# Optimization experiments

Measured on AMD Instinct MI355X. Metric: run time of the kernel, lower is better.

## Reference

```python
import jax, jax.numpy as jnp
import numpy as np

L, N, K, S, V, H = 12, 2048, 8, 4, 50000, 256


def setup_inputs() -> dict:
    key = jax.random.key(0)
    ks = jax.random.split(key, 20)
    tokens1 = jax.random.randint(ks[0], (L, N, S), 0, V, dtype=jnp.int32)
    tokens2 = jax.random.randint(ks[1], (L, N, S), 0, V, dtype=jnp.int32)
    # child indices into previous level's h (0 = zero-init row, -1 = no child)
    idx1 = jax.random.randint(ks[2], (L, N, K), -1, N + 1, dtype=jnp.int32).at[0].set(-1)
    idx2 = jax.random.randint(ks[3], (L, N, K), -1, N + 1, dtype=jnp.int32).at[0].set(-1)
    sc = 0.02
    E = jax.random.normal(ks[4], (V, H), jnp.float32)  # torch.randn init
    lin_W = jax.random.normal(ks[5], (H * S, H), jnp.float32) * sc
    lin_b = jnp.zeros((H,), jnp.float32)
    Uf_W = jax.random.normal(ks[6], (H, H), jnp.float32) * sc
    Uf_b = jnp.zeros((H,), jnp.float32)
    Uiuo_W = jax.random.normal(ks[7], (H, 3 * H), jnp.float32) * sc
    Uiuo_b = jnp.zeros((3 * H,), jnp.float32)
    W_W = jax.random.normal(ks[8], (H, 4 * H), jnp.float32) * sc
    W_b = jnp.zeros((4 * H,), jnp.float32)
    dense_W = jax.random.normal(ks[9], (H, 512), jnp.float32) * sc
    dense_b = jnp.zeros((512,), jnp.float32)
    out_W = jax.random.normal(ks[10], (512, 2), jnp.float32) * sc
    out_b = jnp.zeros((2,), jnp.float32)
    return dict(tokens1=tokens1, idx1=idx1, tokens2=tokens2, idx2=idx2,
                E=E, lin_W=lin_W, lin_b=lin_b, Uf_W=Uf_W, Uf_b=Uf_b,
                Uiuo_W=Uiuo_W, Uiuo_b=Uiuo_b, W_W=W_W, W_b=W_b,
                dense_W=dense_W, dense_b=dense_b, out_W=out_W, out_b=out_b)


def _encode(tokens, idx, E, lin_W, lin_b, Uf_W, Uf_b, Uiuo_W, Uiuo_b, W_W, W_b):
    # TreeEmbeddingLayer: lookup label_size tokens per node, concat, linear
    emb = E[tokens].reshape(L, N, S * H)           # [L,N,S*H]
    x = emb @ lin_W + lin_b                        # [L,N,H]

    def step(carry, inp):
        h_prev, c_prev = carry                     # [N,H]
        xl, il = inp                               # [N,H], [N,K]
        zero = jnp.zeros((1, H), xl.dtype)
        hp = jnp.concatenate([zero, h_prev], 0)    # [N+1,H] (row 0 = init)
        cp = jnp.concatenate([zero, c_prev], 0)
        mask_bool = il != -1
        index = jnp.where(mask_bool, il, 0)
        h = hp[index]                              # [N,K,H] gather child states
        c = cp[index]
        m = mask_bool[..., None].astype(xl.dtype)  # [N,K,1]
        h_sum = jnp.sum(h * m, axis=1)             # [N,H]
        Wx = xl @ W_W + W_b                        # [N,4H]
        Wf, Wi, Wu, Wo = Wx[:, :H], Wx[:, H:2*H], Wx[:, 2*H:3*H], Wx[:, 3*H:]
        fk = jax.nn.sigmoid(Wf[:, None, :] + h @ Uf_W + Uf_b)  # [N,K,H]
        bf = jnp.sum(fk * c * m, axis=1)           # [N,H]
        iuo = h_sum @ Uiuo_W + Uiuo_b              # [N,3H]
        i = jax.nn.sigmoid(iuo[:, :H] + Wi)
        u = jnp.tanh(iuo[:, H:2*H] + Wu)
        o = jax.nn.sigmoid(iuo[:, 2*H:] + Wo)
        nc = i * u + bf
        nh = o * jnp.tanh(nc)
        return (nh, nc), nh

    init = (jnp.zeros((N, H), x.dtype), jnp.zeros((N, H), x.dtype))
    (_, _), hs = jax.lax.scan(step, init, (x, idx))
    # 1 layer with skip connection; hx = last (root) level
    return hs[-1] + x[-1]                          # [N,H]


def reference(tokens1, idx1, tokens2, idx2, E, lin_W, lin_b, Uf_W, Uf_b,
              Uiuo_W, Uiuo_b, W_W, W_b, dense_W, dense_b, out_W, out_b):
    h1 = _encode(tokens1, idx1, E, lin_W, lin_b, Uf_W, Uf_b, Uiuo_W, Uiuo_b, W_W, W_b)
    h2 = _encode(tokens2, idx2, E, lin_W, lin_b, Uf_W, Uf_b, Uiuo_W, Uiuo_b, W_W, W_b)
    abs_dist = jnp.abs(h1 - h2)                    # [N,H]
    x = jnp.tanh(abs_dist @ dense_W + dense_b)     # dropout = identity (eval)
    logits = x @ out_W + out_b                     # [N,2]
    return jax.nn.softmax(logits, axis=-1)
```

## Files before the change

kernel.cpp:

```cpp
#include <hip/hip_runtime.h>

#define LL 12
#define NN 2048
#define KK 8
#define SS 4
#define HH 256
#define LN (LL*NN)
#define VV 50000
#define ZROW 4096
#define SROW 1536

typedef __bf16 bf16_t;
typedef __bf16 bf16x8 __attribute__((ext_vector_type(8)));
typedef __bf16 bf16x4v __attribute__((ext_vector_type(4)));
typedef float f32x4 __attribute__((ext_vector_type(4)));

__device__ __forceinline__ float sigmoidf_(float x) { return 1.f / (1.f + expf(-x)); }

__global__ __launch_bounds__(256) void k_cvtE(const float* __restrict__ src,
                                              bf16_t* __restrict__ dst, int n4)
{
    int i = blockIdx.x * 256 + threadIdx.x;
    const int stride = gridDim.x * 256;
    for (; i < n4; i += stride) {
        const float4 v = ((const float4*)src)[i];
        bf16x4v o;
        o[0] = (bf16_t)v.x; o[1] = (bf16_t)v.y; o[2] = (bf16_t)v.z; o[3] = (bf16_t)v.w;
        ((bf16x4v*)dst)[i] = o;
    }
}

__global__ __launch_bounds__(256) void k_cvtW(
    const float* __restrict__ linW, const float* __restrict__ WW,
    const float* __restrict__ UfW, const float* __restrict__ UiW,
    bf16_t* __restrict__ linWt, bf16_t* __restrict__ WWt,
    bf16_t* __restrict__ UfWt, bf16_t* __restrict__ UiWt)
{
    int i = blockIdx.x * 256 + threadIdx.x;
    if (i < 262144) {
        const int rr = i >> 8, cc = i & 255;
        linWt[(size_t)cc * 1024 + rr] = (bf16_t)linW[i];
        return;
    }
    i -= 262144;
    if (i < 262144) {
        const int rr = i >> 10, cc = i & 1023;
        WWt[(size_t)cc * 256 + rr] = (bf16_t)WW[i];
        return;
    }
    i -= 262144;
    if (i < 65536) {
        const int rr = i >> 8, cc = i & 255;
        UfWt[(size_t)cc * 256 + rr] = (bf16_t)UfW[i];
        return;
    }
    i -= 65536;
    if (i < 196608) {
        const int rr = i / 768, cc = i - rr * 768;
        UiWt[(size_t)cc * 256 + rr] = (bf16_t)UiW[i];
    }
}

__global__ __launch_bounds__(256) void k_zero(float* __restrict__ SA, float* __restrict__ SB)
{
    const int t = threadIdx.x;
    float* a = SA + (size_t)ZROW * 384;
    float* b = SB + (size_t)ZROW * 384;
    for (int i = t; i < 384; i += 256) { a[i] = 0.f; b[i] = 0.f; }
}

__global__ __launch_bounds__(256) void k_embedwx(
    const int* __restrict__ tok1, const int* __restrict__ tok2,
    const bf16_t* __restrict__ Ebf, const bf16_t* __restrict__ linWt,
    const float* __restrict__ linb,
    const bf16_t* __restrict__ WWt, const float* __restrict__ Wb,
    bf16_t* __restrict__ xsm, bf16_t* __restrict__ Wxs)
{
    __shared__ int toff[64][SS];
    __shared__ __align__(16) bf16_t xtile[64 * 256];
    const int t = threadIdx.x;
    const int m0 = blockIdx.x * 64;
    {
        const int lr = t >> 2, s = t & 3;
        const int m = m0 + lr;
        const int e = (m >= LN) ? 1 : 0;
        const int rrow = m - e * LN;
        const int* tok = e ? tok2 : tok1;
        toff[lr][s] = tok[(size_t)rrow * SS + s] * HH;
    }
    __syncthreads();
    const int lane = t & 63, w = t >> 6;
    const int wm = w >> 1, wn = w & 1;
    const int r = lane & 15, kg = lane >> 4;
    const int lr0 = wm * 32 + r, lr1 = lr0 + 16;
    const f32x4 zero = {0.f, 0.f, 0.f, 0.f};

    {
        const bf16_t* bp[8];
        #pragma unroll
        for (int j = 0; j < 8; ++j)
            bp[j] = linWt + (size_t)(wn * 128 + j * 16 + r) * 1024 + kg * 8;
        f32x4 acc[2][8];
        #pragma unroll
        for (int mi = 0; mi < 2; ++mi)
            #pragma unroll
            for (int j = 0; j < 8; ++j) acc[mi][j] = zero;

        for (int k0 = 0; k0 < 1024; k0 += 32) {
            const int s = k0 >> 8, off = (k0 & 255) + kg * 8;
            const bf16x8 a0 = *(const bf16x8*)(Ebf + (size_t)toff[lr0][s] + off);
            const bf16x8 a1 = *(const bf16x8*)(Ebf + (size_t)toff[lr1][s] + off);
            #pragma unroll
            for (int j = 0; j < 8; ++j) {
                const bf16x8 b = *(const bf16x8*)bp[j];
                acc[0][j] = __builtin_amdgcn_mfma_f32_16x16x32_bf16(a0, b, acc[0][j], 0, 0, 0);
                acc[1][j] = __builtin_amdgcn_mfma_f32_16x16x32_bf16(a1, b, acc[1][j], 0, 0, 0);
                bp[j] += 32;
            }
        }
        const int e0 = (m0 >= LN) ? 1 : 0;
        const int lblk = (m0 - e0 * LN) >> 11;
        const int nbase = m0 & (NN - 1);
        const int crowL = wm * 32 + kg * 4;
        #pragma unroll
        for (int j = 0; j < 8; ++j) {
            const int ccol = wn * 128 + j * 16 + r;
            const float bv = linb[ccol];
            #pragma unroll
            for (int mi = 0; mi < 2; ++mi) {
                #pragma unroll
                for (int jj = 0; jj < 4; ++jj) {
                    const int rowL = crowL + mi * 16 + jj;
                    const bf16_t val = (bf16_t)(acc[mi][j][jj] + bv);
                    const int ps = ((ccol >> 3) + rowL) & 31;
                    xtile[rowL * 256 + ps * 8 + (ccol & 7)] = val;
                    if (lblk == LL - 1)
                        xsm[((size_t)e0 * NN + nbase + rowL) * HH + ccol] = val;
                }
            }
        }
    }
    __syncthreads();

    for (int mp = 0; mp < 2; ++mp) {
        for (int nh = 0; nh < 2; ++nh) {
            f32x4 acc2[2][8];
            #pragma unroll
            for (int mi = 0; mi < 2; ++mi)
                #pragma unroll
                for (int nt = 0; nt < 8; ++nt) acc2[mi][nt] = zero;
            for (int k0 = 0; k0 < 8; ++k0) {
                const int row0 = mp * 32 + r, row1 = row0 + 16;
                const int sk = k0 * 4 + kg;
                const bf16x8 a0 = *(const bf16x8*)(xtile + row0 * 256 + ((sk + row0) & 31) * 8);
                const bf16x8 a1 = *(const bf16x8*)(xtile + row1 * 256 + ((sk + row1) & 31) * 8);
                #pragma unroll
                for (int nt = 0; nt < 8; ++nt) {
                    const bf16x8 b = *(const bf16x8*)(WWt +
                        (size_t)(w * 256 + (nh * 8 + nt) * 16 + r) * HH + k0 * 32 + kg * 8);
                    acc2[0][nt] = __builtin_amdgcn_mfma_f32_16x16x32_bf16(a0, b, acc2[0][nt], 0, 0, 0);
                    acc2[1][nt] = __builtin_amdgcn_mfma_f32_16x16x32_bf16(a1, b, acc2[1][nt], 0, 0, 0);
                }
            }
            #pragma unroll
            for (int nt = 0; nt < 8; ++nt) {
                const int col = w * 256 + (nh * 8 + nt) * 16 + r;
                const float bv = Wb[col];
                #pragma unroll
                for (int mi = 0; mi < 2; ++mi) {
                    #pragma unroll
                    for (int jj = 0; jj < 4; ++jj)
                        Wxs[(size_t)(m0 + mp * 32 + mi * 16 + kg * 4 + jj) * 1024 + col] =
                            (bf16_t)(acc2[mi][nt][jj] + bv);
                }
            }
        }
    }
}

__global__ __launch_bounds__(512, 2) void k_step2(
    const int* __restrict__ idx1, const int* __restrict__ idx2, const int l,
    const bf16_t* __restrict__ UfWt, const float* __restrict__ Ufb,
    const bf16_t* __restrict__ UiWt, const float* __restrict__ Uib,
    const bf16_t* __restrict__ Wxs,
    const char* __restrict__ Sprev, char* __restrict__ Snext)
{
    __shared__ __align__(16) bf16_t iuoL[16 * 768];
    __shared__ __align__(16) bf16_t hsumL[16 * 256];

    const int t = threadIdx.x;
    const int bid = blockIdx.x;
    const int x  = bid & 7;
    const int e  = x >> 2;
    const int n0 = ((bid >> 3) * 4 + (x & 3)) * 16;
    const int g0 = e * NN + n0;
    const int lane = t & 63, w = t >> 6;
    const int r = lane & 15, kg = lane >> 4;
    const f32x4 zero = {0.f, 0.f, 0.f, 0.f};

    const int rr = t >> 5, sl = t & 31;
    const int ss = (sl + 4 * (rr & 7)) & 31;

    int ch[KK];
    {
        const int* idxp = (e ? idx2 : idx1) + ((size_t)l * NN + n0 + rr) * KK;
        const int4 i0 = *(const int4*)idxp;
        const int4 i1 = *(const int4*)(idxp + 4);
        ch[0] = i0.x; ch[1] = i0.y; ch[2] = i0.z; ch[3] = i0.w;
        ch[4] = i1.x; ch[5] = i1.y; ch[6] = i1.z; ch[7] = i1.w;
        #pragma unroll
        for (int k = 0; k < KK; ++k)
            ch[k] = (ch[k] >= 1) ? (e * NN + ch[k] - 1) : ZROW;
    }

    const bf16_t* wxp = Wxs + ((size_t)e * LN + (size_t)l * NN + n0 + rr) * 1024;
    const bf16x8 wfv = *(const bf16x8*)(wxp + sl * 8);
    const bf16x8 wiv = *(const bf16x8*)(wxp + 256 + sl * 8);
    const bf16x8 wuv = *(const bf16x8*)(wxp + 512 + sl * 8);
    const bf16x8 wov = *(const bf16x8*)(wxp + 768 + sl * 8);
    bf16x8 hv[KK], fv[KK], cv[KK];
    #pragma unroll
    for (int k = 0; k < KK; ++k) {
        const char* row = Sprev + (size_t)ch[k] * SROW;
        hv[k] = *(const bf16x8*)(row + sl * 16);
        fv[k] = *(const bf16x8*)(row + 512 + sl * 16);
        cv[k] = *(const bf16x8*)(row + 1024 + sl * 16);
    }

    {
        float hs[8] = {0.f, 0.f, 0.f, 0.f, 0.f, 0.f, 0.f, 0.f};
        #pragma unroll
        for (int k = 0; k < KK; ++k) {
            #pragma unroll
            for (int j = 0; j < 8; ++j) hs[j] += (float)hv[k][j];
        }
        bf16x8 o;
        #pragma unroll
        for (int j = 0; j < 8; ++j) o[j] = (bf16_t)hs[j];
        *(bf16x8*)(hsumL + rr * 256 + ss * 8) = o;
    }
    __syncthreads();

    {
        const bf16_t* bu[6];
        #pragma unroll
        for (int j = 0; j < 6; ++j)
            bu[j] = UiWt + (size_t)((6 * w + j) * 16 + r) * HH + kg * 8;
        f32x4 acc[6];
        #pragma unroll
        for (int j = 0; j < 6; ++j) acc[j] = zero;
        for (int k0 = 0; k0 < HH; k0 += 32) {
            const int sa = (((k0 >> 3) + kg) + 4 * (r & 7)) & 31;
            const bf16x8 a = *(const bf16x8*)(hsumL + r * 256 + sa * 8);
            #pragma unroll
            for (int j = 0; j < 6; ++j) {
                const bf16x8 b = *(const bf16x8*)bu[j];
                acc[j] = __builtin_amdgcn_mfma_f32_16x16x32_bf16(a, b, acc[j], 0, 0, 0);
                bu[j] += 32;
            }
        }
        #pragma unroll
        for (int j = 0; j < 6; ++j) {
            const int col = (6 * w + j) * 16 + r;
            const float bv = Uib[col];
            #pragma unroll
            for (int jj = 0; jj < 4; ++jj)
                iuoL[(size_t)(kg * 4 + jj) * 768 + col] = (bf16_t)(acc[j][jj] + bv);
        }
    }

    float ba[8] = {0.f, 0.f, 0.f, 0.f, 0.f, 0.f, 0.f, 0.f};
    {
        float wf[8];
        #pragma unroll
        for (int j = 0; j < 8; ++j) wf[j] = (float)wfv[j];
        #pragma unroll
        for (int k = 0; k < KK; ++k) {
            #pragma unroll
            for (int j = 0; j < 8; ++j) {
                const float fk = sigmoidf_(wf[j] + (float)fv[k][j]);
                ba[j] = fmaf(fk, (float)cv[k][j], ba[j]);
            }
        }
    }
    __syncthreads();

    {
        const bf16x8 iv = *(const bf16x8*)(iuoL + (size_t)rr * 768 + sl * 8);
        const bf16x8 uv = *(const bf16x8*)(iuoL + (size_t)rr * 768 + 256 + sl * 8);
        const bf16x8 ov = *(const bf16x8*)(iuoL + (size_t)rr * 768 + 512 + sl * 8);
        bf16x8 ncb, nhb;
        #pragma unroll
        for (int j = 0; j < 8; ++j) {
            const float ig = sigmoidf_((float)iv[j] + (float)wiv[j]);
            const float ug = tanhf((float)uv[j] + (float)wuv[j]);
            const float og = sigmoidf_((float)ov[j] + (float)wov[j]);
            const float nc = fmaf(ig, ug, ba[j]);
            ncb[j] = (bf16_t)nc;
            nhb[j] = (bf16_t)(og * tanhf(nc));
        }
        char* rowN = Snext + (size_t)(g0 + rr) * SROW;
        *(bf16x8*)(rowN + sl * 16) = nhb;
        *(bf16x8*)(rowN + 1024 + sl * 16) = ncb;
        *(bf16x8*)(hsumL + rr * 256 + ss * 8) = nhb;
    }

    if (l < LL - 1) {
        __syncthreads();
        const int ct0 = 2 * w;
        const bf16_t* bq0 = UfWt + (size_t)(ct0 * 16 + r) * HH + kg * 8;
        const bf16_t* bq1 = bq0 + (size_t)16 * HH;
        f32x4 ac0 = zero, ac1 = zero;
        for (int k0 = 0; k0 < HH; k0 += 32) {
            const int sa = (((k0 >> 3) + kg) + 4 * (r & 7)) & 31;
            const bf16x8 a = *(const bf16x8*)(hsumL + r * 256 + sa * 8);
            const bf16x8 b0 = *(const bf16x8*)bq0;
            const bf16x8 b1 = *(const bf16x8*)bq1;
            ac0 = __builtin_amdgcn_mfma_f32_16x16x32_bf16(a, b0, ac0, 0, 0, 0);
            ac1 = __builtin_amdgcn_mfma_f32_16x16x32_bf16(a, b1, ac1, 0, 0, 0);
            bq0 += 32; bq1 += 32;
        }
        const int c0 = ct0 * 16 + r, c1 = c0 + 16;
        const float bv0 = Ufb[c0], bv1 = Ufb[c1];
        #pragma unroll
        for (int jj = 0; jj < 4; ++jj) {
            bf16_t* fr = (bf16_t*)(Snext + (size_t)(g0 + kg * 4 + jj) * SROW + 512);
            fr[c0] = (bf16_t)(ac0[jj] + bv0);
            fr[c1] = (bf16_t)(ac1[jj] + bv1);
        }
    }
}

__global__ __launch_bounds__(256) void k_final2(
    const char* __restrict__ Sfin, const bf16_t* __restrict__ xsm,
    const float* __restrict__ dW, const float* __restrict__ db,
    const float* __restrict__ oW, const float* __restrict__ ob,
    float* __restrict__ out)
{
    __shared__ __align__(16) float ad[8][HH];
    __shared__ __align__(16) float xx[8][512];
    const int t = threadIdx.x;
    const int n0 = blockIdx.x * 8;
    #pragma unroll
    for (int rr = 0; rr < 8; ++rr) {
        const int n = n0 + rr;
        const float h1 = (float)((const bf16_t*)(Sfin + (size_t)n * SROW))[t]
                       + (float)xsm[(size_t)n * HH + t];
        const float h2 = (float)((const bf16_t*)(Sfin + (size_t)(NN + n) * SROW))[t]
                       + (float)xsm[((size_t)NN + n) * HH + t];
        ad[rr][t] = fabsf(h1 - h2);
    }
    __syncthreads();
    float a0[8], a1[8];
    #pragma unroll
    for (int rr = 0; rr < 8; ++rr) { a0[rr] = 0.f; a1[rr] = 0.f; }
    for (int k = 0; k < HH; k += 4) {
        #pragma unroll
        for (int kk = 0; kk < 4; ++kk) {
            const float b0 = dW[(size_t)(k + kk) * 512 + t];
            const float b1 = dW[(size_t)(k + kk) * 512 + 256 + t];
            #pragma unroll
            for (int rr = 0; rr < 8; ++rr) {
                const float av = ad[rr][k + kk];
                a0[rr] = fmaf(av, b0, a0[rr]);
                a1[rr] = fmaf(av, b1, a1[rr]);
            }
        }
    }
    const float db0 = db[t], db1 = db[256 + t];
    #pragma unroll
    for (int rr = 0; rr < 8; ++rr) {
        xx[rr][t] = tanhf(a0[rr] + db0);
        xx[rr][256 + t] = tanhf(a1[rr] + db1);
    }
    __syncthreads();
    const int w = t >> 6, lane = t & 63;
    for (int rr = w; rr < 8; rr += 4) {
        float p0 = 0.f, p1 = 0.f;
        for (int k = lane; k < 512; k += 64) {
            const float xv = xx[rr][k];
            p0 = fmaf(xv, oW[2 * k + 0], p0);
            p1 = fmaf(xv, oW[2 * k + 1], p1);
        }
        #pragma unroll
        for (int off = 32; off > 0; off >>= 1) {
            p0 += __shfl_down(p0, off);
            p1 += __shfl_down(p1, off);
        }
        if (lane == 0) {
            const float l0 = p0 + ob[0], l1 = p1 + ob[1];
            const float mx = fmaxf(l0, l1);
            const float e0 = expf(l0 - mx), e1 = expf(l1 - mx);
            const float inv = 1.f / (e0 + e1);
            out[(size_t)(n0 + rr) * 2 + 0] = e0 * inv;
            out[(size_t)(n0 + rr) * 2 + 1] = e1 * inv;
        }
    }
}

__global__ __launch_bounds__(256) void k_embed(
    const int* __restrict__ tok1, const int* __restrict__ tok2,
    const bf16_t* __restrict__ Ebf, const bf16_t* __restrict__ linWt,
    const float* __restrict__ linb, bf16_t* __restrict__ xout)
{
    __shared__ int toff[64][SS];
    const int t = threadIdx.x;
    const int m0 = blockIdx.x * 64;
    {
        const int lr = t >> 2, s = t & 3;
        const int m = m0 + lr;
        const int e = (m >= LN) ? 1 : 0;
        const int rrow = m - e * LN;
        const int* tok = e ? tok2 : tok1;
        toff[lr][s] = tok[(size_t)rrow * SS + s] * HH;
    }
    __syncthreads();
    const int lane = t & 63, w = t >> 6;
    const int wm = w >> 1, wn = w & 1;
    const int r = lane & 15, kg = lane >> 4;
    const int lr0 = wm * 32 + r, lr1 = lr0 + 16;
    const bf16_t* bp[8];
    #pragma unroll
    for (int j = 0; j < 8; ++j)
        bp[j] = linWt + (size_t)(wn * 128 + j * 16 + r) * 1024 + kg * 8;
    const f32x4 zero = {0.f, 0.f, 0.f, 0.f};
    f32x4 acc[2][8];
    #pragma unroll
    for (int mi = 0; mi < 2; ++mi)
        #pragma unroll
        for (int j = 0; j < 8; ++j) acc[mi][j] = zero;
    for (int k0 = 0; k0 < 1024; k0 += 32) {
        const int s = k0 >> 8, off = (k0 & 255) + kg * 8;
        const bf16x8 a0 = *(const bf16x8*)(Ebf + (size_t)toff[lr0][s] + off);
        const bf16x8 a1 = *(const bf16x8*)(Ebf + (size_t)toff[lr1][s] + off);
        #pragma unroll
        for (int j = 0; j < 8; ++j) {
            const bf16x8 b = *(const bf16x8*)bp[j];
            acc[0][j] = __builtin_amdgcn_mfma_f32_16x16x32_bf16(a0, b, acc[0][j], 0, 0, 0);
            acc[1][j] = __builtin_amdgcn_mfma_f32_16x16x32_bf16(a1, b, acc[1][j], 0, 0, 0);
            bp[j] += 32;
        }
    }
    const int crow = m0 + wm * 32 + kg * 4;
    #pragma unroll
    for (int j = 0; j < 8; ++j) {
        const int ccol = wn * 128 + j * 16 + r;
        const float bv = linb[ccol];
        #pragma unroll
        for (int mi = 0; mi < 2; ++mi)
            #pragma unroll
            for (int jj = 0; jj < 4; ++jj)
                xout[(size_t)(crow + mi * 16 + jj) * HH + ccol] =
                    (bf16_t)(acc[mi][j][jj] + bv);
    }
}

__global__ __launch_bounds__(512, 2) void k_step(
    const bf16_t* __restrict__ xbf,
    const int* __restrict__ idx1, const int* __restrict__ idx2, const int l,
    const bf16_t* __restrict__ UfWt, const float* __restrict__ Ufb,
    const bf16_t* __restrict__ UiWt, const float* __restrict__ Uib,
    const bf16_t* __restrict__ WWt, const float* __restrict__ Wb,
    const char* __restrict__ Sprev, char* __restrict__ Snext)
{
    __shared__ __align__(16) bf16_t WxL[16 * 1024];
    __shared__ __align__(16) bf16_t iuoL[16 * 768];
    __shared__ __align__(16) bf16_t hsumL[16 * 256];
    const int t = threadIdx.x;
    const int bid = blockIdx.x;
    const int x  = bid & 7;
    const int e  = x >> 2;
    const int n0 = ((bid >> 3) * 4 + (x & 3)) * 16;
    const int g0 = e * NN + n0;
    const int lane = t & 63, w = t >> 6;
    const int r = lane & 15, kg = lane >> 4;
    const f32x4 zero = {0.f, 0.f, 0.f, 0.f};
    const int rr = t >> 5, sl = t & 31;
    const int ss = (sl + 4 * (rr & 7)) & 31;
    int ch[KK];
    {
        const int* idxp = (e ? idx2 : idx1) + ((size_t)l * NN + n0 + rr) * KK;
        const int4 i0 = *(const int4*)idxp;
        const int4 i1 = *(const int4*)(idxp + 4);
        ch[0] = i0.x; ch[1] = i0.y; ch[2] = i0.z; ch[3] = i0.w;
        ch[4] = i1.x; ch[5] = i1.y; ch[6] = i1.z; ch[7] = i1.w;
        #pragma unroll
        for (int k = 0; k < KK; ++k)
            ch[k] = (ch[k] >= 1) ? (e * NN + ch[k] - 1) : ZROW;
    }
    bf16x8 hv[KK];
    #pragma unroll
    for (int k = 0; k < KK; ++k)
        hv[k] = *(const bf16x8*)(Sprev + (size_t)ch[k] * SROW + sl * 16);
    const bf16_t* xrow = xbf + ((size_t)e * LN + (size_t)l * NN + n0 + r) * HH + kg * 8;
    bf16x8 aWx[8];
    #pragma unroll
    for (int k = 0; k < 8; ++k) aWx[k] = *(const bf16x8*)(xrow + k * 32);
    {
        const bf16_t* bw[8];
        #pragma unroll
        for (int j = 0; j < 8; ++j)
            bw[j] = WWt + (size_t)((8 * w + j) * 16 + r) * HH + kg * 8;
        f32x4 acc[8];
        #pragma unroll
        for (int j = 0; j < 8; ++j) acc[j] = zero;
        #pragma unroll
        for (int k = 0; k < 8; ++k) {
            #pragma unroll
            for (int j = 0; j < 8; ++j) {
                const bf16x8 b = *(const bf16x8*)bw[j];
                acc[j] = __builtin_amdgcn_mfma_f32_16x16x32_bf16(aWx[k], b, acc[j], 0, 0, 0);
                bw[j] += 32;
            }
        }
        #pragma unroll
        for (int j = 0; j < 8; ++j) {
            const int col = (8 * w + j) * 16 + r;
            const float bv = Wb[col];
            #pragma unroll
            for (int jj = 0; jj < 4; ++jj)
                WxL[(size_t)(kg * 4 + jj) * 1024 + col] = (bf16_t)(acc[j][jj] + bv);
        }
    }
    {
        float hs[8] = {0.f, 0.f, 0.f, 0.f, 0.f, 0.f, 0.f, 0.f};
        #pragma unroll
        for (int k = 0; k < KK; ++k) {
            #pragma unroll
            for (int j = 0; j < 8; ++j) hs[j] += (float)hv[k][j];
        }
        bf16x8 o;
        #pragma unroll
        for (int j = 0; j < 8; ++j) o[j] = (bf16_t)hs[j];
        *(bf16x8*)(hsumL + rr * 256 + ss * 8) = o;
    }
    __syncthreads();
    bf16x8 cv[KK], fvv[KK];
    #pragma unroll
    for (int k = 0; k < KK; ++k) {
        const char* row = Sprev + (size_t)ch[k] * SROW;
        fvv[k] = *(const bf16x8*)(row + 512 + sl * 16);
        cv[k]  = *(const bf16x8*)(row + 1024 + sl * 16);
    }
    {
        const bf16_t* bu[6];
        #pragma unroll
        for (int j = 0; j < 6; ++j)
            bu[j] = UiWt + (size_t)((6 * w + j) * 16 + r) * HH + kg * 8;
        f32x4 acc[6];
        #pragma unroll
        for (int j = 0; j < 6; ++j) acc[j] = zero;
        for (int k0 = 0; k0 < HH; k0 += 32) {
            const int sa = (((k0 >> 3) + kg) + 4 * (r & 7)) & 31;
            const bf16x8 a = *(const bf16x8*)(hsumL + r * 256 + sa * 8);
            #pragma unroll
            for (int j = 0; j < 6; ++j) {
                const bf16x8 b = *(const bf16x8*)bu[j];
                acc[j] = __builtin_amdgcn_mfma_f32_16x16x32_bf16(a, b, acc[j], 0, 0, 0);
                bu[j] += 32;
            }
        }
        #pragma unroll
        for (int j = 0; j < 6; ++j) {
            const int col = (6 * w + j) * 16 + r;
            const float bv = Uib[col];
            #pragma unroll
            for (int jj = 0; jj < 4; ++jj)
                iuoL[(size_t)(kg * 4 + jj) * 768 + col] = (bf16_t)(acc[j][jj] + bv);
        }
    }
    float ba[8] = {0.f, 0.f, 0.f, 0.f, 0.f, 0.f, 0.f, 0.f};
    {
        float wf[8];
        const bf16x8 wv = *(const bf16x8*)(WxL + (size_t)rr * 1024 + sl * 8);
        #pragma unroll
        for (int j = 0; j < 8; ++j) wf[j] = (float)wv[j];
        #pragma unroll
        for (int k = 0; k < KK; ++k) {
            #pragma unroll
            for (int j = 0; j < 8; ++j) {
                const float fk = sigmoidf_(wf[j] + (float)fvv[k][j]);
                ba[j] = fmaf(fk, (float)cv[k][j], ba[j]);
            }
        }
    }
    __syncthreads();
    {
        const bf16x8 wiv = *(const bf16x8*)(WxL + (size_t)rr * 1024 + 256 + sl * 8);
        const bf16x8 wuv = *(const bf16x8*)(WxL + (size_t)rr * 1024 + 512 + sl * 8);
        const bf16x8 wov = *(const bf16x8*)(WxL + (size_t)rr * 1024 + 768 + sl * 8);
        const bf16x8 iv  = *(const bf16x8*)(iuoL + (size_t)rr * 768 + sl * 8);
        const bf16x8 uv  = *(const bf16x8*)(iuoL + (size_t)rr * 768 + 256 + sl * 8);
        const bf16x8 ov  = *(const bf16x8*)(iuoL + (size_t)rr * 768 + 512 + sl * 8);
        bf16x8 ncb, nhb;
        #pragma unroll
        for (int j = 0; j < 8; ++j) {
            const float ig = sigmoidf_((float)iv[j] + (float)wiv[j]);
            const float ug = tanhf((float)uv[j] + (float)wuv[j]);
            const float og = sigmoidf_((float)ov[j] + (float)wov[j]);
            const float nc = fmaf(ig, ug, ba[j]);
            ncb[j] = (bf16_t)nc;
            nhb[j] = (bf16_t)(og * tanhf(nc));
        }
        char* rowN = Snext + (size_t)(g0 + rr) * SROW;
        *(bf16x8*)(rowN + sl * 16) = nhb;
        *(bf16x8*)(rowN + 1024 + sl * 16) = ncb;
        *(bf16x8*)(hsumL + rr * 256 + ss * 8) = nhb;
    }
    if (l < LL - 1) {
        __syncthreads();
        const int ct0 = 2 * w;
        const bf16_t* bq0 = UfWt + (size_t)(ct0 * 16 + r) * HH + kg * 8;
        const bf16_t* bq1 = bq0 + (size_t)16 * HH;
        f32x4 ac0 = zero, ac1 = zero;
        for (int k0 = 0; k0 < HH; k0 += 32) {
            const int sa = (((k0 >> 3) + kg) + 4 * (r & 7)) & 31;
            const bf16x8 a = *(const bf16x8*)(hsumL + r * 256 + sa * 8);
            const bf16x8 b0 = *(const bf16x8*)bq0;
            const bf16x8 b1 = *(const bf16x8*)bq1;
            ac0 = __builtin_amdgcn_mfma_f32_16x16x32_bf16(a, b0, ac0, 0, 0, 0);
            ac1 = __builtin_amdgcn_mfma_f32_16x16x32_bf16(a, b1, ac1, 0, 0, 0);
            bq0 += 32; bq1 += 32;
        }
        const int c0 = ct0 * 16 + r, c1 = c0 + 16;
        const float bv0 = Ufb[c0], bv1 = Ufb[c1];
        #pragma unroll
        for (int jj = 0; jj < 4; ++jj) {
            bf16_t* fr = (bf16_t*)(Snext + (size_t)(g0 + kg * 4 + jj) * SROW + 512);
            fr[c0] = (bf16_t)(ac0[jj] + bv0);
            fr[c1] = (bf16_t)(ac1[jj] + bv1);
        }
    }
}

__global__ __launch_bounds__(256) void k_final(
    const char* __restrict__ Sfin, const bf16_t* __restrict__ xbf,
    const float* __restrict__ dW, const float* __restrict__ db,
    const float* __restrict__ oW, const float* __restrict__ ob,
    float* __restrict__ out)
{
    __shared__ __align__(16) float ad[8][HH];
    __shared__ __align__(16) float xx[8][512];
    const int t = threadIdx.x;
    const int n0 = blockIdx.x * 8;
    const size_t xoff1 = (size_t)(LL - 1) * NN * HH;
    const size_t xoff2 = (size_t)LN * HH + xoff1;
    #pragma unroll
    for (int rr = 0; rr < 8; ++rr) {
        const int n = n0 + rr;
        const float h1 = (float)((const bf16_t*)(Sfin + (size_t)n * SROW))[t]
                       + (float)xbf[xoff1 + (size_t)n * HH + t];
        const float h2 = (float)((const bf16_t*)(Sfin + (size_t)(NN + n) * SROW))[t]
                       + (float)xbf[xoff2 + (size_t)n * HH + t];
        ad[rr][t] = fabsf(h1 - h2);
    }
    __syncthreads();
    float a0[8], a1[8];
    #pragma unroll
    for (int rr = 0; rr < 8; ++rr) { a0[rr] = 0.f; a1[rr] = 0.f; }
    for (int k = 0; k < HH; k += 4) {
        #pragma unroll
        for (int kk = 0; kk < 4; ++kk) {
            const float b0 = dW[(size_t)(k + kk) * 512 + t];
            const float b1 = dW[(size_t)(k + kk) * 512 + 256 + t];
            #pragma unroll
            for (int rr = 0; rr < 8; ++rr) {
                const float av = ad[rr][k + kk];
                a0[rr] = fmaf(av, b0, a0[rr]);
                a1[rr] = fmaf(av, b1, a1[rr]);
            }
        }
    }
    const float db0 = db[t], db1 = db[256 + t];
    #pragma unroll
    for (int rr = 0; rr < 8; ++rr) {
        xx[rr][t] = tanhf(a0[rr] + db0);
        xx[rr][256 + t] = tanhf(a1[rr] + db1);
    }
    __syncthreads();
    const int w = t >> 6, lane = t & 63;
    for (int rr = w; rr < 8; rr += 4) {
        float p0 = 0.f, p1 = 0.f;
        for (int k = lane; k < 512; k += 64) {
            const float xv = xx[rr][k];
            p0 = fmaf(xv, oW[2 * k + 0], p0);
            p1 = fmaf(xv, oW[2 * k + 1], p1);
        }
        #pragma unroll
        for (int off = 32; off > 0; off >>= 1) {
            p0 += __shfl_down(p0, off);
            p1 += __shfl_down(p1, off);
        }
        if (lane == 0) {
            const float l0 = p0 + ob[0], l1 = p1 + ob[1];
            const float mx = fmaxf(l0, l1);
            const float e0 = expf(l0 - mx), e1 = expf(l1 - mx);
            const float inv = 1.f / (e0 + e1);
            out[(size_t)(n0 + rr) * 2 + 0] = e0 * inv;
            out[(size_t)(n0 + rr) * 2 + 1] = e1 * inv;
        }
    }
}

extern "C" void kernel_launch(void* const* d_in, const int* in_sizes, int n_in,
                              void* d_out, int out_size, void* d_ws, size_t ws_size,
                              hipStream_t stream) {
    (void)in_sizes; (void)n_in; (void)out_size;
    const int*   tok1 = (const int*)d_in[0];
    const int*   idx1 = (const int*)d_in[1];
    const int*   tok2 = (const int*)d_in[2];
    const int*   idx2 = (const int*)d_in[3];
    const float* E    = (const float*)d_in[4];
    const float* linW = (const float*)d_in[5];
    const float* linb = (const float*)d_in[6];
    const float* UfW  = (const float*)d_in[7];
    const float* Ufb  = (const float*)d_in[8];
    const float* UiW  = (const float*)d_in[9];
    const float* Uib  = (const float*)d_in[10];
    const float* WW   = (const float*)d_in[11];
    const float* Wb   = (const float*)d_in[12];
    const float* dW   = (const float*)d_in[13];
    const float* db   = (const float*)d_in[14];
    const float* oW   = (const float*)d_in[15];
    const float* ob   = (const float*)d_in[16];
    float* out = (float*)d_out;

    const size_t NEED = 100663296ull + 25600000ull + 2097152ull + 1572864ull;

    if (ws_size >= NEED) {
        bf16_t* Wxs = (bf16_t*)d_ws;
        char*   uni = (char*)d_ws + 100663296;
        bf16_t* Ebf = (bf16_t*)uni;
        char*   SA  = uni;
        char*   SB  = uni + 6292992;
        bf16_t* xsm = (bf16_t*)(uni + 25600000);
        bf16_t* linWt = (bf16_t*)(uni + 25600000 + 2097152);
        bf16_t* WWt   = linWt + (size_t)262144;
        bf16_t* UfWt  = WWt   + (size_t)262144;
        bf16_t* UiWt  = UfWt  + (size_t)65536;

        k_cvtE<<<2048, 256, 0, stream>>>(E, Ebf, VV * HH / 4);
        k_cvtW<<<3072, 256, 0, stream>>>(linW, WW, UfW, UiW, linWt, WWt, UfWt, UiWt);
        k_embedwx<<<768, 256, 0, stream>>>(tok1, tok2, Ebf, linWt, linb, WWt, Wb, xsm, Wxs);
        k_zero<<<1, 256, 0, stream>>>((float*)SA, (float*)SB);

        char *Sp = SA, *Sn = SB;
        for (int l = 0; l < LL; ++l) {
            k_step2<<<256, 512, 0, stream>>>(idx1, idx2, l, UfWt, Ufb, UiWt, Uib,
                                             Wxs, Sp, Sn);
            char* ts = Sp; Sp = Sn; Sn = ts;
        }
        k_final2<<<NN / 8, 256, 0, stream>>>(Sp, xsm, dW, db, oW, ob, out);
    } else {
        bf16_t* xbf = (bf16_t*)d_ws;
        char*   uni = (char*)(xbf + (size_t)12582912);
        bf16_t* Ebf = (bf16_t*)uni;
        char*   SA  = uni;
        char*   SB  = uni + 6292992;
        bf16_t* linWt = (bf16_t*)(uni + 25600000);
        bf16_t* WWt   = linWt + (size_t)262144;
        bf16_t* UfWt  = WWt   + (size_t)262144;
        bf16_t* UiWt  = UfWt  + (size_t)65536;

        k_cvtE<<<2048, 256, 0, stream>>>(E, Ebf, VV * HH / 4);
        k_cvtW<<<3072, 256, 0, stream>>>(linW, WW, UfW, UiW, linWt, WWt, UfWt, UiWt);
        k_embed<<<768, 256, 0, stream>>>(tok1, tok2, Ebf, linWt, linb, xbf);
        k_zero<<<1, 256, 0, stream>>>((float*)SA, (float*)SB);

        char *Sp = SA, *Sn = SB;
        for (int l = 0; l < LL; ++l) {
            k_step<<<256, 512, 0, stream>>>(xbf, idx1, idx2, l,
                                            UfWt, Ufb, UiWt, Uib, WWt, Wb, Sp, Sn);
            char* ts = Sp; Sp = Sn; Sn = ts;
        }
        k_final<<<NN / 8, 256, 0, stream>>>(Sp, xbf, dW, db, oW, ob, out);
    }
}
```

Baseline: 698.8 us.

## Split fused embedding and Wx GEMM into separate kernels with a wider grid

The fused embed+Wx kernel is split in two. `k_embed` now writes the embedded x rows to global memory. A new `k_wx` kernel then computes the x·W projection over a 4×768 grid of 64×256 tiles. The old kernel ran the whole 64×1024 Wx projection serially inside each of 768 blocks from a shared-memory tile; spreading it across more blocks is meant to raise occupancy and parallelism. The cost is an extra global round-trip of x and one more launch, and the workspace is re-laid out so buffers whose lifetimes do not overlap share memory.

```diff
diff --git a/kernel.cpp b/kernel.cpp
--- a/kernel.cpp
+++ b/kernel.cpp
@@ -69,15 +69,13 @@
     for (int i = t; i < 384; i += 256) { a[i] = 0.f; b[i] = 0.f; }
 }
 
-__global__ __launch_bounds__(256) void k_embedwx(
+__global__ __launch_bounds__(256) void k_embed(
     const int* __restrict__ tok1, const int* __restrict__ tok2,
     const bf16_t* __restrict__ Ebf, const bf16_t* __restrict__ linWt,
-    const float* __restrict__ linb,
-    const bf16_t* __restrict__ WWt, const float* __restrict__ Wb,
-    bf16_t* __restrict__ xsm, bf16_t* __restrict__ Wxs)
+    const float* __restrict__ linb, bf16_t* __restrict__ xout,
+    bf16_t* __restrict__ xsm)
 {
     __shared__ int toff[64][SS];
-    __shared__ __align__(16) bf16_t xtile[64 * 256];
     const int t = threadIdx.x;
     const int m0 = blockIdx.x * 64;
     {
@@ -93,88 +91,98 @@
     const int wm = w >> 1, wn = w & 1;
     const int r = lane & 15, kg = lane >> 4;
     const int lr0 = wm * 32 + r, lr1 = lr0 + 16;
+    const bf16_t* bp[8];
+    #pragma unroll
+    for (int j = 0; j < 8; ++j)
+        bp[j] = linWt + (size_t)(wn * 128 + j * 16 + r) * 1024 + kg * 8;
+
     const f32x4 zero = {0.f, 0.f, 0.f, 0.f};
-
-    {
-        const bf16_t* bp[8];
-        #pragma unroll
-        for (int j = 0; j < 8; ++j)
-            bp[j] = linWt + (size_t)(wn * 128 + j * 16 + r) * 1024 + kg * 8;
-        f32x4 acc[2][8];
+    f32x4 acc[2][8];
+    #pragma unroll
+    for (int mi = 0; mi < 2; ++mi)
+        #pragma unroll
+        for (int j = 0; j < 8; ++j) acc[mi][j] = zero;
+
+    for (int k0 = 0; k0 < 1024; k0 += 32) {
+        const int s = k0 >> 8, off = (k0 & 255) + kg * 8;
+        const bf16x8 a0 = *(const bf16x8*)(Ebf + (size_t)toff[lr0][s] + off);
+        const bf16x8 a1 = *(const bf16x8*)(Ebf + (size_t)toff[lr1][s] + off);
+        #pragma unroll
+        for (int j = 0; j < 8; ++j) {
+            const bf16x8 b = *(const bf16x8*)bp[j];
+            acc[0][j] = __builtin_amdgcn_mfma_f32_16x16x32_bf16(a0, b, acc[0][j], 0, 0, 0);
+            acc[1][j] = __builtin_amdgcn_mfma_f32_16x16x32_bf16(a1, b, acc[1][j], 0, 0, 0);
+            bp[j] += 32;
+        }
+    }
+    const int e0 = (m0 >= LN) ? 1 : 0;
+    const int lblk = (m0 - e0 * LN) >> 11;
+    const int nbase = m0 & (NN - 1);
+    const int crow = m0 + wm * 32 + kg * 4;
+    const int lrow = wm * 32 + kg * 4;
+    #pragma unroll
+    for (int j = 0; j < 8; ++j) {
+        const int ccol = wn * 128 + j * 16 + r;
+        const float bv = linb[ccol];
         #pragma unroll
         for (int mi = 0; mi < 2; ++mi)
             #pragma unroll
-            for (int j = 0; j < 8; ++j) acc[mi][j] = zero;
-
-        for (int k0 = 0; k0 < 1024; k0 += 32) {
-            const int s = k0 >> 8, off = (k0 & 255) + kg * 8;
-            const bf16x8 a0 = *(const bf16x8*)(Ebf + (size_t)toff[lr0][s] + off);
-            const bf16x8 a1 = *(const bf16x8*)(Ebf + (size_t)toff[lr1][s] + off);
-            #pragma unroll
-            for (int j = 0; j < 8; ++j) {
-                const bf16x8 b = *(const bf16x8*)bp[j];
-                acc[0][j] = __builtin_amdgcn_mfma_f32_16x16x32_bf16(a0, b, acc[0][j], 0, 0, 0);
-                acc[1][j] = __builtin_amdgcn_mfma_f32_16x16x32_bf16(a1, b, acc[1][j], 0, 0, 0);
-                bp[j] += 32;
+            for (int jj = 0; jj < 4; ++jj) {
+                const bf16_t val = (bf16_t)(acc[mi][j][jj] + bv);
+                xout[(size_t)(crow + mi * 16 + jj) * HH + ccol] = val;
+                if (lblk == LL - 1)
+                    xsm[((size_t)e0 * NN + nbase + lrow + mi * 16 + jj) * HH + ccol] = val;
             }
-        }
-        const int e0 = (m0 >= LN) ? 1 : 0;
-        const int lblk = (m0 - e0 * LN) >> 11;
-        const int nbase = m0 & (NN - 1);
-        const int crowL = wm * 32 + kg * 4;
+    }
+}
+
+__global__ __launch_bounds__(256) void k_wx(
+    const bf16_t* __restrict__ xbf, const bf16_t* __restrict__ WWt,
+    const float* __restrict__ Wb, bf16_t* __restrict__ Wxs)
+{
+    const int n0 = blockIdx.x * 256;
+    const int m0 = blockIdx.y * 64;
+    const int t = threadIdx.x;
+    const int lane = t & 63, w = t >> 6;
+    const int wm = w >> 1, wn = w & 1;
+    const int r = lane & 15, kg = lane >> 4;
+    const int lr0 = wm * 32 + r, lr1 = lr0 + 16;
+    const bf16_t* ap0 = xbf + (size_t)(m0 + lr0) * HH + kg * 8;
+    const bf16_t* ap1 = xbf + (size_t)(m0 + lr1) * HH + kg * 8;
+    const bf16_t* bp[8];
+    #pragma unroll
+    for (int j = 0; j < 8; ++j)
+        bp[j] = WWt + (size_t)(n0 + wn * 128 + j * 16 + r) * HH + kg * 8;
+
+    const f32x4 zero = {0.f, 0.f, 0.f, 0.f};
+    f32x4 acc[2][8];
+    #pragma unroll
+    for (int mi = 0; mi < 2; ++mi)
+        #pragma unroll
+        for (int j = 0; j < 8; ++j) acc[mi][j] = zero;
+
+    for (int k0 = 0; k0 < HH; k0 += 32) {
+        const bf16x8 a0 = *(const bf16x8*)(ap0 + k0);
+        const bf16x8 a1 = *(const bf16x8*)(ap1 + k0);
         #pragma unroll
         for (int j = 0; j < 8; ++j) {
-            const int ccol = wn * 128 + j * 16 + r;
-            const float bv = linb[ccol];
-            #pragma unroll
-            for (int mi = 0; mi < 2; ++mi) {
-                #pragma unroll
-                for (int jj = 0; jj < 4; ++jj) {
-                    const int rowL = crowL + mi * 16 + jj;
-                    const bf16_t val = (bf16_t)(acc[mi][j][jj] + bv);
-                    const int ps = ((ccol >> 3) + rowL) & 31;
-                    xtile[rowL * 256 + ps * 8 + (ccol & 7)] = val;
-                    if (lblk == LL - 1)
-                        xsm[((size_t)e0 * NN + nbase + rowL) * HH + ccol] = val;
-                }
-            }
-        }
-    }
-    __syncthreads();
-
-    for (int mp = 0; mp < 2; ++mp) {
-        for (int nh = 0; nh < 2; ++nh) {
-            f32x4 acc2[2][8];
-            #pragma unroll
-            for (int mi = 0; mi < 2; ++mi)
-                #pragma unroll
-                for (int nt = 0; nt < 8; ++nt) acc2[mi][nt] = zero;
-            for (int k0 = 0; k0 < 8; ++k0) {
-                const int row0 = mp * 32 + r, row1 = row0 + 16;
-                const int sk = k0 * 4 + kg;
-                const bf16x8 a0 = *(const bf16x8*)(xtile + row0 * 256 + ((sk + row0) & 31) * 8);
-                const bf16x8 a1 = *(const bf16x8*)(xtile + row1 * 256 + ((sk + row1) & 31) * 8);
-                #pragma unroll
-                for (int nt = 0; nt < 8; ++nt) {
-                    const bf16x8 b = *(const bf16x8*)(WWt +
-                        (size_t)(w * 256 + (nh * 8 + nt) * 16 + r) * HH + k0 * 32 + kg * 8);
-                    acc2[0][nt] = __builtin_amdgcn_mfma_f32_16x16x32_bf16(a0, b, acc2[0][nt], 0, 0, 0);
-                    acc2[1][nt] = __builtin_amdgcn_mfma_f32_16x16x32_bf16(a1, b, acc2[1][nt], 0, 0, 0);
-                }
-            }
-            #pragma unroll
-            for (int nt = 0; nt < 8; ++nt) {
-                const int col = w * 256 + (nh * 8 + nt) * 16 + r;
-                const float bv = Wb[col];
-                #pragma unroll
-                for (int mi = 0; mi < 2; ++mi) {
-                    #pragma unroll
-                    for (int jj = 0; jj < 4; ++jj)
-                        Wxs[(size_t)(m0 + mp * 32 + mi * 16 + kg * 4 + jj) * 1024 + col] =
-                            (bf16_t)(acc2[mi][nt][jj] + bv);
-                }
-            }
-        }
+            const bf16x8 b = *(const bf16x8*)bp[j];
+            acc[0][j] = __builtin_amdgcn_mfma_f32_16x16x32_bf16(a0, b, acc[0][j], 0, 0, 0);
+            acc[1][j] = __builtin_amdgcn_mfma_f32_16x16x32_bf16(a1, b, acc[1][j], 0, 0, 0);
+            bp[j] += 32;
+        }
+    }
+    const int crow = m0 + wm * 32 + kg * 4;
+    #pragma unroll
+    for (int j = 0; j < 8; ++j) {
+        const int ccol = n0 + wn * 128 + j * 16 + r;
+        const float bv = Wb[ccol];
+        #pragma unroll
+        for (int mi = 0; mi < 2; ++mi)
+            #pragma unroll
+            for (int jj = 0; jj < 4; ++jj)
+                Wxs[(size_t)(crow + mi * 16 + jj) * 1024 + ccol] =
+                    (bf16_t)(acc[mi][j][jj] + bv);
     }
 }
 
@@ -395,63 +403,6 @@
             out[(size_t)(n0 + rr) * 2 + 0] = e0 * inv;
             out[(size_t)(n0 + rr) * 2 + 1] = e1 * inv;
         }
-    }
-}
-
-__global__ __launch_bounds__(256) void k_embed(
-    const int* __restrict__ tok1, const int* __restrict__ tok2,
-    const bf16_t* __restrict__ Ebf, const bf16_t* __restrict__ linWt,
-    const float* __restrict__ linb, bf16_t* __restrict__ xout)
-{
-    __shared__ int toff[64][SS];
-    const int t = threadIdx.x;
-    const int m0 = blockIdx.x * 64;
-    {
-        const int lr = t >> 2, s = t & 3;
-        const int m = m0 + lr;
-        const int e = (m >= LN) ? 1 : 0;
-        const int rrow = m - e * LN;
-        const int* tok = e ? tok2 : tok1;
-        toff[lr][s] = tok[(size_t)rrow * SS + s] * HH;
-    }
-    __syncthreads();
-    const int lane = t & 63, w = t >> 6;
-    const int wm = w >> 1, wn = w & 1;
-    const int r = lane & 15, kg = lane >> 4;
-    const int lr0 = wm * 32 + r, lr1 = lr0 + 16;
-    const bf16_t* bp[8];
-    #pragma unroll
-    for (int j = 0; j < 8; ++j)
-        bp[j] = linWt + (size_t)(wn * 128 + j * 16 + r) * 1024 + kg * 8;
-    const f32x4 zero = {0.f, 0.f, 0.f, 0.f};
-    f32x4 acc[2][8];
-    #pragma unroll
-    for (int mi = 0; mi < 2; ++mi)
-        #pragma unroll
-        for (int j = 0; j < 8; ++j) acc[mi][j] = zero;
-    for (int k0 = 0; k0 < 1024; k0 += 32) {
-        const int s = k0 >> 8, off = (k0 & 255) + kg * 8;
-        const bf16x8 a0 = *(const bf16x8*)(Ebf + (size_t)toff[lr0][s] + off);
-        const bf16x8 a1 = *(const bf16x8*)(Ebf + (size_t)toff[lr1][s] + off);
-        #pragma unroll
-        for (int j = 0; j < 8; ++j) {
-            const bf16x8 b = *(const bf16x8*)bp[j];
-            acc[0][j] = __builtin_amdgcn_mfma_f32_16x16x32_bf16(a0, b, acc[0][j], 0, 0, 0);
-            acc[1][j] = __builtin_amdgcn_mfma_f32_16x16x32_bf16(a1, b, acc[1][j], 0, 0, 0);
-            bp[j] += 32;
-        }
-    }
-    const int crow = m0 + wm * 32 + kg * 4;
-    #pragma unroll
-    for (int j = 0; j < 8; ++j) {
-        const int ccol = wn * 128 + j * 16 + r;
-        const float bv = linb[ccol];
-        #pragma unroll
-        for (int mi = 0; mi < 2; ++mi)
-            #pragma unroll
-            for (int jj = 0; jj < 4; ++jj)
-                xout[(size_t)(crow + mi * 16 + jj) * HH + ccol] =
-                    (bf16_t)(acc[mi][j][jj] + bv);
     }
 }
 
@@ -725,23 +676,25 @@
     const float* ob   = (const float*)d_in[16];
     float* out = (float*)d_out;
 
-    const size_t NEED = 100663296ull + 25600000ull + 2097152ull + 1572864ull;
+    const size_t NEED = 129499136ull;
 
     if (ws_size >= NEED) {
-        bf16_t* Wxs = (bf16_t*)d_ws;
-        char*   uni = (char*)d_ws + 100663296;
-        bf16_t* Ebf = (bf16_t*)uni;
-        char*   SA  = uni;
-        char*   SB  = uni + 6292992;
-        bf16_t* xsm = (bf16_t*)(uni + 25600000);
-        bf16_t* linWt = (bf16_t*)(uni + 25600000 + 2097152);
+        bf16_t* xbf = (bf16_t*)d_ws;
+        char*   SA  = (char*)d_ws;
+        char*   SB  = (char*)d_ws + 6292992;
+        char*   r2  = (char*)d_ws + 25165824;
+        bf16_t* Wxs = (bf16_t*)r2;
+        bf16_t* Ebf = (bf16_t*)r2;
+        bf16_t* xsm = (bf16_t*)(r2 + 100663296);
+        bf16_t* linWt = (bf16_t*)(r2 + 100663296 + 2097152);
         bf16_t* WWt   = linWt + (size_t)262144;
         bf16_t* UfWt  = WWt   + (size_t)262144;
         bf16_t* UiWt  = UfWt  + (size_t)65536;
 
         k_cvtE<<<2048, 256, 0, stream>>>(E, Ebf, VV * HH / 4);
         k_cvtW<<<3072, 256, 0, stream>>>(linW, WW, UfW, UiW, linWt, WWt, UfWt, UiWt);
-        k_embedwx<<<768, 256, 0, stream>>>(tok1, tok2, Ebf, linWt, linb, WWt, Wb, xsm, Wxs);
+        k_embed<<<768, 256, 0, stream>>>(tok1, tok2, Ebf, linWt, linb, xbf, xsm);
+        k_wx<<<dim3(4, 768), 256, 0, stream>>>(xbf, WWt, Wb, Wxs);
         k_zero<<<1, 256, 0, stream>>>((float*)SA, (float*)SB);
 
         char *Sp = SA, *Sn = SB;
@@ -761,10 +714,13 @@
         bf16_t* WWt   = linWt + (size_t)262144;
         bf16_t* UfWt  = WWt   + (size_t)262144;
         bf16_t* UiWt  = UfWt  + (size_t)65536;
+        bf16_t* xsm_f = (bf16_t*)(uni + 25600000 - 4194304);
+        (void)xsm_f;
 
         k_cvtE<<<2048, 256, 0, stream>>>(E, Ebf, VV * HH / 4);
         k_cvtW<<<3072, 256, 0, stream>>>(linW, WW, UfW, UiW, linWt, WWt, UfWt, UiWt);
-        k_embed<<<768, 256, 0, stream>>>(tok1, tok2, Ebf, linWt, linb, xbf);
+        k_embed<<<768, 256, 0, stream>>>(tok1, tok2, Ebf, linWt, linb, xbf,
+                                         xbf + (size_t)(LL - 1) * NN * HH);
         k_zero<<<1, 256, 0, stream>>>((float*)SA, (float*)SB);
 
         char *Sp = SA, *Sn = SB;
```

After: 657.1 us. 1.06x faster.
